# Optimization experiments

Hardware: AMD Instinct MI355X
Metric: run time of the kernel (lower is better)

## Reference

```python
import jax, jax.numpy as jnp
import numpy as np

N = 100_000      # points
F = 64           # feature dim
B = 4            # graphs in batch
POOL_RAD = 0.2   # voxel size
D = 8            # static upper bound on voxels per spatial dim
M_MAX = 1024     # static upper bound on number of nonempty clusters


def setup_inputs() -> dict:
    key = jax.random.key(0)
    k1, k2, k3 = jax.random.split(key, 3)
    pos = jax.random.uniform(k1, (N, 3), dtype=jnp.float32)
    x = jax.random.normal(k2, (N, F), dtype=jnp.float32)
    batch = jnp.sort(jax.random.randint(k3, (N,), 0, B)).astype(jnp.int32)
    return {"pos": pos, "x": x, "batch": batch}


def reference(pos, x, batch):
    batch = batch.astype(jnp.int32)
    rad = jnp.asarray(POOL_RAD, pos.dtype)
    # --- voxel_grid clustering (start = min - rad/2 as in the torch module) ---
    start = pos.min(axis=0) - rad * 0.5
    coords = jnp.clip(jnp.floor((pos - start) / rad).astype(jnp.int32), 0, D - 1)  # [N,3]
    vox = ((batch * D + coords[:, 0]) * D + coords[:, 1]) * D + coords[:, 2]       # [N]
    V = B * D * D * D
    # --- consecutive_cluster + scatter mean of positions ---
    ones = jnp.ones((pos.shape[0],), pos.dtype)
    counts = jax.ops.segment_sum(ones, vox, num_segments=V)       # [V]
    sum_pos = jax.ops.segment_sum(pos, vox, num_segments=V)       # [V,3]
    nonempty = counts > 0
    # compact nonempty voxels to static M_MAX slots (padding duplicates voxel idx 0;
    # argmin tie-breaking to the first index keeps duplicates inert)
    idx = jnp.nonzero(nonempty, size=M_MAX, fill_value=0)[0]      # [M_MAX]
    valid = jnp.arange(M_MAX) < jnp.sum(nonempty)                 # [M_MAX]
    centroids = sum_pos[idx] / jnp.maximum(counts[idx], 1.0)[:, None]  # [M_MAX,3]
    new_batch = idx // (D * D * D)                                # [M_MAX]
    # --- nearest: assign each point to nearest cluster centroid in same graph ---
    d2 = (jnp.sum(pos * pos, axis=1)[:, None]
          - 2.0 * pos @ centroids.T
          + jnp.sum(centroids * centroids, axis=1)[None, :])      # [N, M_MAX]
    big = jnp.asarray(1e30, pos.dtype)
    d2 = jnp.where((batch[:, None] == new_batch[None, :]) & valid[None, :], d2, big)
    assign = jnp.argmin(d2, axis=1)                               # [N]
    # --- scatter max of features into clusters (empty clusters -> 0, as in PyG) ---
    x_pool = jax.ops.segment_max(x, assign, num_segments=M_MAX)   # [M_MAX, F]
    x_pool = jnp.where(jnp.isfinite(x_pool), x_pool, jnp.zeros_like(x_pool))
    return x_pool, centroids, new_batch, valid
```

## Files before the change

kernel.cpp:

```cpp
#include <hip/hip_runtime.h>
#include <stdint.h>

#define DGRID 8
#define NVOX  2048
#define NBATCH 4
#define MMAX  1024
#define FDIM  64
#define CHUNKP 256
#define GRP   20

__device__ __forceinline__ unsigned encf(float f){
  unsigned u = __float_as_uint(f);
  return (u & 0x80000000u) ? ~u : (u | 0x80000000u);
}
__device__ __forceinline__ float decf(unsigned e){
  unsigned u = (e & 0x80000000u) ? (e ^ 0x80000000u) : ~e;
  return __uint_as_float(u);
}


__global__ __launch_bounds__(256) void k_minpart(const float* __restrict__ pos,
    int N, unsigned* __restrict__ bmin, int* __restrict__ counts,
    int* __restrict__ clustCnt, int* __restrict__ clustRank){
  if (blockIdx.x < 8) counts[blockIdx.x * 256 + threadIdx.x] = 0;
  else if (blockIdx.x < 12) clustCnt[(blockIdx.x - 8) * 256 + threadIdx.x] = 0;
  else if (blockIdx.x < 16) clustRank[(blockIdx.x - 12) * 256 + threadIdx.x] = 0;
  unsigned m0 = 0xFFFFFFFFu, m1 = 0xFFFFFFFFu, m2 = 0xFFFFFFFFu;
  int stride = gridDim.x * blockDim.x;
  for (int i = blockIdx.x * blockDim.x + threadIdx.x; i < N; i += stride){
    unsigned e0 = encf(pos[3*i+0]); if (e0 < m0) m0 = e0;
    unsigned e1 = encf(pos[3*i+1]); if (e1 < m1) m1 = e1;
    unsigned e2 = encf(pos[3*i+2]); if (e2 < m2) m2 = e2;
  }
  #pragma unroll
  for (int off = 32; off > 0; off >>= 1){
    unsigned t0 = __shfl_down(m0, off); if (t0 < m0) m0 = t0;
    unsigned t1 = __shfl_down(m1, off); if (t1 < m1) m1 = t1;
    unsigned t2 = __shfl_down(m2, off); if (t2 < m2) m2 = t2;
  }
  __shared__ unsigned sm[4][3];
  int wv = threadIdx.x >> 6, lane = threadIdx.x & 63;
  if (lane == 0){ sm[wv][0] = m0; sm[wv][1] = m1; sm[wv][2] = m2; }
  __syncthreads();
  if (threadIdx.x == 0){
    unsigned a0 = sm[0][0], a1 = sm[0][1], a2 = sm[0][2];
    for (int k = 1; k < 4; k++){
      if (sm[k][0] < a0) a0 = sm[k][0];
      if (sm[k][1] < a1) a1 = sm[k][1];
      if (sm[k][2] < a2) a2 = sm[k][2];
    }
    bmin[blockIdx.x*3+0] = a0;
    bmin[blockIdx.x*3+1] = a1;
    bmin[blockIdx.x*3+2] = a2;
  }
}

__global__ __launch_bounds__(256) void k_vox_hist(const float* __restrict__ pos,
    const int* __restrict__ batch, int N, const unsigned* __restrict__ bmin,
    int* __restrict__ vox, int* __restrict__ chunkHist){
  __shared__ int h[NVOX];
  __shared__ unsigned smin[3];
  for (int t = threadIdx.x; t < NVOX; t += 256) h[t] = 0;
  if (threadIdx.x < 64){
    unsigned a0 = bmin[threadIdx.x*3+0];
    unsigned a1 = bmin[threadIdx.x*3+1];
    unsigned a2 = bmin[threadIdx.x*3+2];
    #pragma unroll
    for (int off = 32; off > 0; off >>= 1){
      unsigned t0 = __shfl_down(a0, off); if (t0 < a0) a0 = t0;
      unsigned t1 = __shfl_down(a1, off); if (t1 < a1) a1 = t1;
      unsigned t2 = __shfl_down(a2, off); if (t2 < a2) a2 = t2;
    }
    if (threadIdx.x == 0){ smin[0] = a0; smin[1] = a1; smin[2] = a2; }
  }
  __syncthreads();
  int c = blockIdx.x;
  int i = c * CHUNKP + threadIdx.x;
  if (i < N){
    float s0 = __fsub_rn(decf(smin[0]), 0.1f);
    float s1 = __fsub_rn(decf(smin[1]), 0.1f);
    float s2 = __fsub_rn(decf(smin[2]), 0.1f);
    float q0 = __fdiv_rn(__fsub_rn(pos[3*i+0], s0), 0.2f);
    float q1 = __fdiv_rn(__fsub_rn(pos[3*i+1], s1), 0.2f);
    float q2 = __fdiv_rn(__fsub_rn(pos[3*i+2], s2), 0.2f);
    int c0 = (int)floorf(q0); c0 = c0 < 0 ? 0 : (c0 > DGRID-1 ? DGRID-1 : c0);
    int c1 = (int)floorf(q1); c1 = c1 < 0 ? 0 : (c1 > DGRID-1 ? DGRID-1 : c1);
    int c2 = (int)floorf(q2); c2 = c2 < 0 ? 0 : (c2 > DGRID-1 ? DGRID-1 : c2);
    int v = ((batch[i]*DGRID + c0)*DGRID + c1)*DGRID + c2;
    vox[i] = v;
    atomicAdd(&h[v], 1);
  }
  __syncthreads();
  for (int t = threadIdx.x; t < NVOX; t += 256)
    chunkHist[c * NVOX + t] = h[t];
}

__global__ __launch_bounds__(256) void k_gsum(int nchunks, int ngroups,
    const int* __restrict__ chunkHist, int* __restrict__ gsum){
  int g = blockIdx.x >> 3;
  int v = (blockIdx.x & 7) * 256 + threadIdx.x;
  if (g >= ngroups) return;
  int c0 = g * GRP, c1 = min(nchunks, c0 + GRP);
  int s = 0;
  for (int c = c0; c < c1; c++) s += chunkHist[c * NVOX + v];
  gsum[g * NVOX + v] = s;
}

__global__ __launch_bounds__(256) void k_gscan(int ngroups,
    int* __restrict__ gsum, int* __restrict__ counts){
  int v = blockIdx.x * 256 + threadIdx.x;
  if (v >= NVOX) return;
  int run = 0;
  for (int g = 0; g < ngroups; g++){
    int t = gsum[g * NVOX + v];
    gsum[g * NVOX + v] = run;
    run += t;
  }
  counts[v] = run;
}

__global__ __launch_bounds__(256) void k_scatter(const float* __restrict__ pos,
    const int* __restrict__ vox, int N, const int* __restrict__ chunkHist,
    const int* __restrict__ gsum, const int* __restrict__ counts,
    int* Mout, int* batchStartC, int* __restrict__ idxOfCluster,
    int* __restrict__ voxBaseG, float* __restrict__ pos_sorted){
  __shared__ int sBase[NVOX];
  __shared__ int rowCnt[4][NVOX];
  int c = blockIdx.x;
  int wv = threadIdx.x >> 6, lane = threadIdx.x & 63;
  if (wv == 0){
    int cs[32];
    int ne = 0, tot = 0;
    #pragma unroll
    for (int j = 0; j < 32; j++){
      int cc2 = counts[lane*32 + j];
      cs[j] = cc2; ne += (cc2 > 0) ? 1 : 0; tot += cc2;
    }
    int inc = ne, incT = tot;
    #pragma unroll
    for (int off = 1; off < 64; off <<= 1){
      int t  = __shfl_up(inc,  off);
      int tt = __shfl_up(incT, off);
      if (lane >= off){ inc += t; incT += tt; }
    }
    int exne = inc - ne, exT = incT - tot;
    int run = exne, bb = exT;
    #pragma unroll
    for (int j = 0; j < 32; j++){
      sBase[lane*32 + j] = bb;
      if (c == 0) voxBaseG[lane*32 + j] = bb;
      bb += cs[j];
      if (cs[j] > 0){
        if (c == 0 && run < MMAX) idxOfCluster[run] = lane*32 + j;
        run++;
      }
    }
    if (c == 0){
      int M = __shfl(run, 63);
      for (int m = M + lane; m < MMAX; m += 64) idxOfCluster[m] = 0;
      int ex0  = __shfl(exne, 0),  ex16 = __shfl(exne, 16);
      int ex32 = __shfl(exne, 32), ex48 = __shfl(exne, 48);
      if (lane == 0){
        Mout[0] = M;
        batchStartC[0] = ex0;  batchStartC[1] = ex16;
        batchStartC[2] = ex32; batchStartC[3] = ex48;
        batchStartC[NBATCH] = (M < MMAX) ? M : MMAX;
      }
    }
  } else {
    for (int t = threadIdx.x - 64; t < 4*NVOX; t += 192)
      ((int*)rowCnt)[t] = 0;
  }
  __syncthreads();
  {
    int g = c / GRP, cg0 = g * GRP;
    for (int t = threadIdx.x; t < NVOX; t += 256){
      int b = sBase[t] + gsum[g * NVOX + t];
      for (int cc = cg0; cc < c; cc++) b += chunkHist[cc * NVOX + t];
      sBase[t] = b;
    }
  }
  __syncthreads();
  int i = c * CHUNKP + threadIdx.x;
  bool valid = i < N;
  int v = valid ? vox[i] : -1;
  float px = 0.f, py = 0.f, pz = 0.f;
  if (valid){ px = pos[3*i+0]; py = pos[3*i+1]; pz = pos[3*i+2]; }
  int rank = 0, cnt = 0;
  #pragma unroll 8
  for (int j = 0; j < 64; j++){
    int vj = __shfl(v, j);
    if (vj == v){
      cnt++;
      if (j < lane) rank++;
    }
  }
  if (valid && rank == 0) rowCnt[wv][v] = cnt;
  __syncthreads();
  if (valid){
    int pre = 0;
    for (int rr = 0; rr < wv; rr++) pre += rowCnt[rr][v];
    int dst = sBase[v] + pre + rank;
    pos_sorted[3*dst+0] = px;
    pos_sorted[3*dst+1] = py;
    pos_sorted[3*dst+2] = pz;
  }
}

__global__ __launch_bounds__(64) void k_sum2cent(const float* __restrict__ pos_sorted,
    const int* __restrict__ voxBase, const int* __restrict__ counts,
    float4* __restrict__ centv){
  int v = blockIdx.x * 64 + threadIdx.x;
  if (v >= NVOX) return;
  int lo = voxBase[v], cnt = counts[v];
  const float* p = pos_sorted + 3*(size_t)lo;
  float sx = 0.f, sy = 0.f, sz = 0.f;
  int k = 0;
  for (; k + 4 <= cnt; k += 4){
    float a0 = p[0],  a1 = p[1],  a2 = p[2];
    float b0 = p[3],  b1 = p[4],  b2 = p[5];
    float c0 = p[6],  c1 = p[7],  c2 = p[8];
    float d0 = p[9],  d1 = p[10], d2 = p[11];
    sx = __fadd_rn(__fadd_rn(__fadd_rn(__fadd_rn(sx, a0), b0), c0), d0);
    sy = __fadd_rn(__fadd_rn(__fadd_rn(__fadd_rn(sy, a1), b1), c1), d1);
    sz = __fadd_rn(__fadd_rn(__fadd_rn(__fadd_rn(sz, a2), b2), c2), d2);
    p += 12;
  }
  for (; k < cnt; k++){
    sx = __fadd_rn(sx, p[0]);
    sy = __fadd_rn(sy, p[1]);
    sz = __fadd_rn(sz, p[2]);
    p += 3;
  }
  float den = fmaxf((float)cnt, 1.0f);
  float cx = __fdiv_rn(sx, den);
  float cy = __fdiv_rn(sy, den);
  float cz = __fdiv_rn(sz, den);
  float c2 = __fadd_rn(__fadd_rn(__fmul_rn(cx,cx), __fmul_rn(cy,cy)), __fmul_rn(cz,cz));
  centv[v] = make_float4(cx, cy, cz, c2);
}

__global__ __launch_bounds__(256) void k_argmin2(const float* __restrict__ pos,
    const int* __restrict__ batch, int N, const float4* __restrict__ centv,
    const int* __restrict__ idxOfCluster, const int* __restrict__ Mout,
    const int* __restrict__ batchStartC, int* __restrict__ assign,
    int* __restrict__ clustCnt, float* __restrict__ outC,
    float* __restrict__ outNB, float* __restrict__ outValid){
  __shared__ float4 sc[MMAX];
  __shared__ int h[MMAX];
  for (int m = threadIdx.x; m < MMAX; m += 256){
    sc[m] = centv[idxOfCluster[m]];
    h[m] = 0;
  }
  __syncthreads();
  if (blockIdx.x == 0){
    int M = Mout[0];
    for (int m = threadIdx.x; m < MMAX; m += 256){
      float4 cc = sc[m];
      outC[3*m+0] = cc.x; outC[3*m+1] = cc.y; outC[3*m+2] = cc.z;
      outNB[m] = (float)(idxOfCluster[m] >> 9);
      outValid[m] = (m < M) ? 1.0f : 0.0f;
    }
  }
  int i = blockIdx.x * 256 + threadIdx.x;
  if (i < N){
    float px = pos[3*i+0], py = pos[3*i+1], pz = pos[3*i+2];
    float p2 = __fadd_rn(__fadd_rn(__fmul_rn(px,px), __fmul_rn(py,py)), __fmul_rn(pz,pz));
    int b = batch[i];
    int mlo = batchStartC[b], mhi = batchStartC[b+1];
    float best = 3.402823466e+38f;
    int bm = mlo;
    for (int m = mlo; m < mhi; m++){
      float4 cc = sc[m];
      float dot = __fadd_rn(__fadd_rn(__fmul_rn(px,cc.x), __fmul_rn(py,cc.y)),
                            __fmul_rn(pz,cc.z));
      float d2  = __fadd_rn(__fsub_rn(p2, __fmul_rn(2.0f, dot)), cc.w);
      if (d2 < best){ best = d2; bm = m; }
    }
    assign[i] = bm;
    atomicAdd(&h[bm], 1);
  }
  __syncthreads();
  for (int t = threadIdx.x; t < MMAX; t += 256){
    int c = h[t];
    if (c > 0) atomicAdd(&clustCnt[t], c);
  }
}

__global__ __launch_bounds__(256) void k_scatter2s(const int* __restrict__ assign,
    int N, const int* __restrict__ clustCnt, int* __restrict__ clustRank,
    int* __restrict__ clustBaseG, int* __restrict__ idx_sorted){
  __shared__ int cb[MMAX];
  int wv = threadIdx.x >> 6, lane = threadIdx.x & 63;
  if (wv == 0){
    int cs[16]; int tot = 0;
    #pragma unroll
    for (int j = 0; j < 16; j++){ cs[j] = clustCnt[lane*16 + j]; tot += cs[j]; }
    int inc = tot;
    #pragma unroll
    for (int off = 1; off < 64; off <<= 1){
      int t = __shfl_up(inc, off);
      if (lane >= off) inc += t;
    }
    int bb = inc - tot;
    #pragma unroll
    for (int j = 0; j < 16; j++){
      cb[lane*16 + j] = bb;
      if (blockIdx.x == 0) clustBaseG[lane*16 + j] = bb;
      bb += cs[j];
    }
  }
  __syncthreads();
  int i = blockIdx.x * 256 + threadIdx.x;
  if (i >= N) return;
  int m = assign[i];
  int r = atomicAdd(&clustRank[m], 1);
  idx_sorted[cb[m] + r] = i;
}

__global__ __launch_bounds__(256) void k_xmax(const float* __restrict__ x,
    const int* __restrict__ idx_sorted, const int* __restrict__ clustBase,
    const int* __restrict__ clustCnt, float* __restrict__ outX){
  int w = blockIdx.x * 4 + (threadIdx.x >> 6);
  int lane = threadIdx.x & 63;
  if (w >= MMAX) return;
  int lo = clustBase[w], cnt = clustCnt[w];
  float mx = -3.402823466e+38f;
  int k = 0;
  for (; k + 4 <= cnt; k += 4){
    int r0 = idx_sorted[lo+k+0], r1 = idx_sorted[lo+k+1];
    int r2 = idx_sorted[lo+k+2], r3 = idx_sorted[lo+k+3];
    float a = x[(size_t)r0 * FDIM + lane];
    float b = x[(size_t)r1 * FDIM + lane];
    float c = x[(size_t)r2 * FDIM + lane];
    float d = x[(size_t)r3 * FDIM + lane];
    mx = fmaxf(mx, fmaxf(fmaxf(a, b), fmaxf(c, d)));
  }
  for (; k < cnt; k++){
    int r0 = idx_sorted[lo+k];
    mx = fmaxf(mx, x[(size_t)r0 * FDIM + lane]);
  }
  outX[w * FDIM + lane] = (cnt > 0) ? mx : 0.0f;
}


__global__ __launch_bounds__(256) void k_init(unsigned* startEnc, int* batchCnt){
  int t = threadIdx.x;
  if (t < 3) startEnc[t] = 0xFFFFFFFFu;
  if (t < NBATCH) batchCnt[t] = 0;
}

__global__ __launch_bounds__(256) void k_min_hist(const float* __restrict__ pos,
    const int* __restrict__ batch, int N, unsigned* startEnc, int* batchCnt){
  __shared__ int sbin[NBATCH];
  if (threadIdx.x < NBATCH) sbin[threadIdx.x] = 0;
  __syncthreads();
  unsigned m0 = 0xFFFFFFFFu, m1 = 0xFFFFFFFFu, m2 = 0xFFFFFFFFu;
  int stride = gridDim.x * blockDim.x;
  for (int i = blockIdx.x * blockDim.x + threadIdx.x; i < N; i += stride){
    unsigned e0 = encf(pos[3*i+0]); if (e0 < m0) m0 = e0;
    unsigned e1 = encf(pos[3*i+1]); if (e1 < m1) m1 = e1;
    unsigned e2 = encf(pos[3*i+2]); if (e2 < m2) m2 = e2;
    atomicAdd(&sbin[batch[i]], 1);
  }
  #pragma unroll
  for (int off = 32; off > 0; off >>= 1){
    unsigned t0 = __shfl_down(m0, off); if (t0 < m0) m0 = t0;
    unsigned t1 = __shfl_down(m1, off); if (t1 < m1) m1 = t1;
    unsigned t2 = __shfl_down(m2, off); if (t2 < m2) m2 = t2;
  }
  if ((threadIdx.x & 63) == 0){
    atomicMin(&startEnc[0], m0);
    atomicMin(&startEnc[1], m1);
    atomicMin(&startEnc[2], m2);
  }
  __syncthreads();
  if (threadIdx.x < NBATCH) atomicAdd(&batchCnt[threadIdx.x], sbin[threadIdx.x]);
}

__global__ __launch_bounds__(256) void k_vox(const float* __restrict__ pos,
    const int* __restrict__ batch, int N, const unsigned* __restrict__ startEnc,
    int* __restrict__ vox, int* __restrict__ counts){
  int i = blockIdx.x * blockDim.x + threadIdx.x;
  if (i >= N) return;
  float s0 = __fsub_rn(decf(startEnc[0]), 0.1f);
  float s1 = __fsub_rn(decf(startEnc[1]), 0.1f);
  float s2 = __fsub_rn(decf(startEnc[2]), 0.1f);
  float q0 = __fdiv_rn(__fsub_rn(pos[3*i+0], s0), 0.2f);
  float q1 = __fdiv_rn(__fsub_rn(pos[3*i+1], s1), 0.2f);
  float q2 = __fdiv_rn(__fsub_rn(pos[3*i+2], s2), 0.2f);
  int c0 = (int)floorf(q0); c0 = c0 < 0 ? 0 : (c0 > DGRID-1 ? DGRID-1 : c0);
  int c1 = (int)floorf(q1); c1 = c1 < 0 ? 0 : (c1 > DGRID-1 ? DGRID-1 : c1);
  int c2 = (int)floorf(q2); c2 = c2 < 0 ? 0 : (c2 > DGRID-1 ? DGRID-1 : c2);
  int v = ((batch[i]*DGRID + c0)*DGRID + c1)*DGRID + c2;
  vox[i] = v;
  atomicAdd(&counts[v], 1);
}

__global__ __launch_bounds__(64) void k_scan_old(const int* __restrict__ counts,
    const int* __restrict__ batchCnt, int* batchPtr, int* Mout,
    int* batchStartC, int* __restrict__ idxOfCluster, int* __restrict__ voxBase){
  int lane = threadIdx.x;
  int cs[32];
  int ne = 0, tot = 0;
  #pragma unroll
  for (int j = 0; j < 32; j++){
    int c = counts[lane*32 + j];
    cs[j] = c;
    ne += (c > 0) ? 1 : 0;
    tot += c;
  }
  int inc = ne, incT = tot;
  #pragma unroll
  for (int off = 1; off < 64; off <<= 1){
    int t  = __shfl_up(inc,  off);
    int tt = __shfl_up(incT, off);
    if (lane >= off){ inc += t; incT += tt; }
  }
  int exne = inc - ne;
  int bb   = incT - tot;
  int run = exne;
  #pragma unroll
  for (int j = 0; j < 32; j++){
    voxBase[lane*32 + j] = bb;
    bb += cs[j];
    if (cs[j] > 0){
      if (run < MMAX) idxOfCluster[run] = lane*32 + j;
      run++;
    }
  }
  int M = __shfl(run, 63);
  for (int m = M + lane; m < MMAX; m += 64) idxOfCluster[m] = 0;
  int ex0  = __shfl(exne, 0);
  int ex16 = __shfl(exne, 16);
  int ex32 = __shfl(exne, 32);
  int ex48 = __shfl(exne, 48);
  if (lane == 0){
    Mout[0] = M;
    int acc = 0;
    for (int b = 0; b < NBATCH; b++){ batchPtr[b] = acc; acc += batchCnt[b]; }
    batchPtr[NBATCH] = acc;
    batchStartC[0] = ex0;  batchStartC[1] = ex16;
    batchStartC[2] = ex32; batchStartC[3] = ex48;
    batchStartC[NBATCH] = (M < MMAX) ? M : MMAX;
  }
}

__global__ __launch_bounds__(64) void k_sum(const float* __restrict__ pos,
    const int* __restrict__ vox, const int* __restrict__ counts,
    const int* __restrict__ batchPtr, float* __restrict__ sum_pos){
  int v = blockIdx.x * 64 + threadIdx.x;
  if (v >= NVOX) return;
  int b = v >> 9;
  int lo = batchPtr[b], hi = batchPtr[b+1];
  float sx = 0.f, sy = 0.f, sz = 0.f;
  if (counts[v] > 0){
    for (int i = lo; i < hi; i++){
      if (vox[i] == v){
        sx = __fadd_rn(sx, pos[3*i+0]);
        sy = __fadd_rn(sy, pos[3*i+1]);
        sz = __fadd_rn(sz, pos[3*i+2]);
      }
    }
  }
  sum_pos[3*v+0] = sx;
  sum_pos[3*v+1] = sy;
  sum_pos[3*v+2] = sz;
}

__global__ __launch_bounds__(256) void k_cent(const float* __restrict__ sum_pos,
    const int* __restrict__ counts, const int* __restrict__ idxOfCluster,
    const int* __restrict__ Mout, float4* __restrict__ cent4,
    float* __restrict__ outC, float* __restrict__ outNB, float* __restrict__ outValid){
  int m = blockIdx.x * blockDim.x + threadIdx.x;
  if (m >= MMAX) return;
  int M = Mout[0];
  int v = idxOfCluster[m];
  float den = fmaxf((float)counts[v], 1.0f);
  float cx = __fdiv_rn(sum_pos[3*v+0], den);
  float cy = __fdiv_rn(sum_pos[3*v+1], den);
  float cz = __fdiv_rn(sum_pos[3*v+2], den);
  float c2 = __fadd_rn(__fadd_rn(__fmul_rn(cx,cx), __fmul_rn(cy,cy)), __fmul_rn(cz,cz));
  cent4[m] = make_float4(cx, cy, cz, c2);
  outC[3*m+0] = cx; outC[3*m+1] = cy; outC[3*m+2] = cz;
  outNB[m] = (float)(v >> 9);
  outValid[m] = (m < M) ? 1.0f : 0.0f;
}

__global__ __launch_bounds__(256) void k_assign_slow(const float* __restrict__ pos,
    const float* __restrict__ x, const int* __restrict__ batch, int N,
    const float4* __restrict__ cent4, const int* __restrict__ batchStartC,
    unsigned* __restrict__ encMax){
  __shared__ float4 sc[MMAX];
  for (int m = threadIdx.x; m < MMAX; m += blockDim.x) sc[m] = cent4[m];
  __syncthreads();
  int i = blockIdx.x * blockDim.x + threadIdx.x;
  if (i >= N) return;
  float px = pos[3*i+0], py = pos[3*i+1], pz = pos[3*i+2];
  float p2 = __fadd_rn(__fadd_rn(__fmul_rn(px,px), __fmul_rn(py,py)), __fmul_rn(pz,pz));
  int b = batch[i];
  int mlo = batchStartC[b], mhi = batchStartC[b+1];
  float best = 3.402823466e+38f;
  int bm = mlo;
  for (int m = mlo; m < mhi; m++){
    float4 c = sc[m];
    float dot = __fadd_rn(__fadd_rn(__fmul_rn(px,c.x), __fmul_rn(py,c.y)),
                          __fmul_rn(pz,c.z));
    float d2  = __fadd_rn(__fsub_rn(p2, __fmul_rn(2.0f, dot)), c.w);
    if (d2 < best){ best = d2; bm = m; }
  }
  unsigned* dst = encMax + bm * FDIM;
  const float4* xi = (const float4*)(x + (size_t)i * FDIM);
  #pragma unroll
  for (int f4 = 0; f4 < FDIM/4; f4++){
    float4 xv = xi[f4];
    atomicMax(&dst[4*f4+0], encf(xv.x));
    atomicMax(&dst[4*f4+1], encf(xv.y));
    atomicMax(&dst[4*f4+2], encf(xv.z));
    atomicMax(&dst[4*f4+3], encf(xv.w));
  }
}
__global__ __launch_bounds__(256) void k_decode(const unsigned* __restrict__ encMax,
    float* __restrict__ outX){
  int t = blockIdx.x * blockDim.x + threadIdx.x;
  if (t >= MMAX * FDIM) return;
  unsigned e = encMax[t];
  outX[t] = (e == 0u) ? 0.0f : decf(e);
}


extern "C" void kernel_launch(void* const* d_in, const int* in_sizes, int n_in,
                              void* d_out, int out_size, void* d_ws, size_t ws_size,
                              hipStream_t stream){
  const float* pos   = (const float*)d_in[0];
  const float* x     = (const float*)d_in[1];
  const int*   batch = (const int*)d_in[2];
  const int N = in_sizes[2];

  char* w = (char*)d_ws;
  unsigned* bmin         = (unsigned*)(w + 0);
  unsigned* startEnc     = (unsigned*)(w + 768);
  int*      batchCnt     = (int*)(w + 784);
  int*      batchPtr     = (int*)(w + 800);
  int*      Mout         = (int*)(w + 832);
  int*      batchStartC  = (int*)(w + 848);
  int*      counts       = (int*)(w + 896);
  int*      voxBaseG     = (int*)(w + 9088);
  float*    sum_pos      = (float*)(w + 17280);
  int*      idxOfCluster = (int*)(w + 41856);
  float4*   cent4        = (float4*)(w + 45952);
  int*      clustCnt     = (int*)(w + 62336);
  int*      clustBaseG   = (int*)(w + 66432);
  int*      clustRank    = (int*)(w + 70528);
  float4*   centv        = (float4*)(w + 74624);
  unsigned* encMax       = (unsigned*)(w + 107392);
  int*      gsum         = (int*)(w + 107392);
  int*      vox          = (int*)(w + 369536);
  size_t voxEnd = 369536 + (size_t)N * 4;
  size_t chOff  = (voxEnd + 15) & ~(size_t)15;

  int nchunks = (N + CHUNKP - 1) / CHUNKP;
  int ngroups = (nchunks + GRP - 1) / GRP;
  size_t psOff = chOff + (size_t)nchunks * NVOX * 4;
  size_t need  = psOff + (size_t)N * 3 * 4;
  const bool fast = (ws_size >= need) && (ngroups <= 32);

  int*   chunkHist  = (int*)(w + chOff);
  float* pos_sorted = (float*)(w + psOff);
  int* assign     = (int*)pos_sorted;
  int* idx_sorted = (int*)pos_sorted + N;

  float* outX     = (float*)d_out;
  float* outC     = outX + MMAX * FDIM;
  float* outNB    = outC + MMAX * 3;
  float* outValid = outNB + MMAX;

  const int nb = (N + 255) / 256;
  if (fast){
    k_minpart<<<64, 256, 0, stream>>>(pos, N, bmin, counts, clustCnt, clustRank);
    k_vox_hist<<<nchunks, 256, 0, stream>>>(pos, batch, N, bmin, vox, chunkHist);
    k_gsum<<<ngroups * 8, 256, 0, stream>>>(nchunks, ngroups, chunkHist, gsum);
    k_gscan<<<NVOX / 256, 256, 0, stream>>>(ngroups, gsum, counts);
    k_scatter<<<nchunks, 256, 0, stream>>>(pos, vox, N, chunkHist, gsum, counts,
                                           Mout, batchStartC, idxOfCluster,
                                           voxBaseG, pos_sorted);
    k_sum2cent<<<NVOX / 64, 64, 0, stream>>>(pos_sorted, voxBaseG, counts, centv);
    k_argmin2<<<nb, 256, 0, stream>>>(pos, batch, N, centv, idxOfCluster, Mout,
                                      batchStartC, assign, clustCnt,
                                      outC, outNB, outValid);
    k_scatter2s<<<nb, 256, 0, stream>>>(assign, N, clustCnt, clustRank,
                                        clustBaseG, idx_sorted);
    k_xmax<<<MMAX / 4, 256, 0, stream>>>(x, idx_sorted, clustBaseG, clustCnt, outX);
  } else {
    k_init<<<1, 256, 0, stream>>>(startEnc, batchCnt);
    hipMemsetAsync(counts, 0, NVOX * 4, stream);
    hipMemsetAsync(encMax, 0, MMAX * FDIM * 4, stream);
    k_min_hist<<<256, 256, 0, stream>>>(pos, batch, N, startEnc, batchCnt);
    k_vox<<<nb, 256, 0, stream>>>(pos, batch, N, startEnc, vox, counts);
    k_scan_old<<<1, 64, 0, stream>>>(counts, batchCnt, batchPtr, Mout, batchStartC,
                                     idxOfCluster, voxBaseG);
    k_sum<<<(NVOX + 63) / 64, 64, 0, stream>>>(pos, vox, counts, batchPtr, sum_pos);
    k_cent<<<MMAX / 256, 256, 0, stream>>>(sum_pos, counts, idxOfCluster, Mout,
                                           cent4, outC, outNB, outValid);
    k_assign_slow<<<nb, 256, 0, stream>>>(pos, x, batch, N, cent4, batchStartC, encMax);
    k_decode<<<(MMAX * FDIM + 255) / 256, 256, 0, stream>>>(encMax, outX);
  }
}
```

Measured before the change: 149.6 us.

## Recompute voxel ids in scatter and fold group scan into gsum atomics

Drops the per-point vox array: the histogram kernel no longer writes it, and the scatter kernel recomputes voxel indices from pos, batch and the partial minima. The separate k_gscan launch is removed. k_gsum now accumulates total counts with global atomics, and each scatter block sums the preceding group totals itself. This removes one kernel launch and a round trip of N ints through global memory, at the cost of duplicated voxel arithmetic and an O(ngroups) loop per voxel in every scatter block. It relies on counts being zeroed by k_minpart before k_gsum runs.

```diff
diff --git a/kernel.cpp b/kernel.cpp
--- a/kernel.cpp
+++ b/kernel.cpp
@@ -55,9 +55,9 @@
   }
 }
 
-__global__ __launch_bounds__(256) void k_vox_hist(const float* __restrict__ pos,
+__global__ __launch_bounds__(256) void k_chist(const float* __restrict__ pos,
     const int* __restrict__ batch, int N, const unsigned* __restrict__ bmin,
-    int* __restrict__ vox, int* __restrict__ chunkHist){
+    int* __restrict__ chunkHist){
   __shared__ int h[NVOX];
   __shared__ unsigned smin[3];
   for (int t = threadIdx.x; t < NVOX; t += 256) h[t] = 0;
@@ -87,7 +87,6 @@
     int c1 = (int)floorf(q1); c1 = c1 < 0 ? 0 : (c1 > DGRID-1 ? DGRID-1 : c1);
     int c2 = (int)floorf(q2); c2 = c2 < 0 ? 0 : (c2 > DGRID-1 ? DGRID-1 : c2);
     int v = ((batch[i]*DGRID + c0)*DGRID + c1)*DGRID + c2;
-    vox[i] = v;
     atomicAdd(&h[v], 1);
   }
   __syncthreads();
@@ -96,7 +95,8 @@
 }
 
 __global__ __launch_bounds__(256) void k_gsum(int nchunks, int ngroups,
-    const int* __restrict__ chunkHist, int* __restrict__ gsum){
+    const int* __restrict__ chunkHist, int* __restrict__ gsum,
+    int* __restrict__ counts){
   int g = blockIdx.x >> 3;
   int v = (blockIdx.x & 7) * 256 + threadIdx.x;
   if (g >= ngroups) return;
@@ -104,28 +104,18 @@
   int s = 0;
   for (int c = c0; c < c1; c++) s += chunkHist[c * NVOX + v];
   gsum[g * NVOX + v] = s;
-}
-
-__global__ __launch_bounds__(256) void k_gscan(int ngroups,
-    int* __restrict__ gsum, int* __restrict__ counts){
-  int v = blockIdx.x * 256 + threadIdx.x;
-  if (v >= NVOX) return;
-  int run = 0;
-  for (int g = 0; g < ngroups; g++){
-    int t = gsum[g * NVOX + v];
-    gsum[g * NVOX + v] = run;
-    run += t;
-  }
-  counts[v] = run;
+  if (s > 0) atomicAdd(&counts[v], s);
 }
 
 __global__ __launch_bounds__(256) void k_scatter(const float* __restrict__ pos,
-    const int* __restrict__ vox, int N, const int* __restrict__ chunkHist,
+    const int* __restrict__ batch, int N, const int* __restrict__ chunkHist,
     const int* __restrict__ gsum, const int* __restrict__ counts,
+    const unsigned* __restrict__ bmin,
     int* Mout, int* batchStartC, int* __restrict__ idxOfCluster,
     int* __restrict__ voxBaseG, float* __restrict__ pos_sorted){
   __shared__ int sBase[NVOX];
   __shared__ int rowCnt[4][NVOX];
+  __shared__ unsigned smin[3];
   int c = blockIdx.x;
   int wv = threadIdx.x >> 6, lane = threadIdx.x & 63;
   if (wv == 0){
@@ -168,6 +158,18 @@
       }
     }
   } else {
+    if (wv == 1){
+      unsigned a0 = bmin[lane*3+0];
+      unsigned a1 = bmin[lane*3+1];
+      unsigned a2 = bmin[lane*3+2];
+      #pragma unroll
+      for (int off = 32; off > 0; off >>= 1){
+        unsigned t0 = __shfl_down(a0, off); if (t0 < a0) a0 = t0;
+        unsigned t1 = __shfl_down(a1, off); if (t1 < a1) a1 = t1;
+        unsigned t2 = __shfl_down(a2, off); if (t2 < a2) a2 = t2;
+      }
+      if (lane == 0){ smin[0] = a0; smin[1] = a1; smin[2] = a2; }
+    }
     for (int t = threadIdx.x - 64; t < 4*NVOX; t += 192)
       ((int*)rowCnt)[t] = 0;
   }
@@ -175,7 +177,8 @@
   {
     int g = c / GRP, cg0 = g * GRP;
     for (int t = threadIdx.x; t < NVOX; t += 256){
-      int b = sBase[t] + gsum[g * NVOX + t];
+      int b = sBase[t];
+      for (int gg = 0; gg < g; gg++) b += gsum[gg * NVOX + t];
       for (int cc = cg0; cc < c; cc++) b += chunkHist[cc * NVOX + t];
       sBase[t] = b;
     }
@@ -183,9 +186,21 @@
   __syncthreads();
   int i = c * CHUNKP + threadIdx.x;
   bool valid = i < N;
-  int v = valid ? vox[i] : -1;
+  int v = -1;
   float px = 0.f, py = 0.f, pz = 0.f;
-  if (valid){ px = pos[3*i+0]; py = pos[3*i+1]; pz = pos[3*i+2]; }
+  if (valid){
+    px = pos[3*i+0]; py = pos[3*i+1]; pz = pos[3*i+2];
+    float s0 = __fsub_rn(decf(smin[0]), 0.1f);
+    float s1 = __fsub_rn(decf(smin[1]), 0.1f);
+    float s2 = __fsub_rn(decf(smin[2]), 0.1f);
+    float q0 = __fdiv_rn(__fsub_rn(px, s0), 0.2f);
+    float q1 = __fdiv_rn(__fsub_rn(py, s1), 0.2f);
+    float q2 = __fdiv_rn(__fsub_rn(pz, s2), 0.2f);
+    int c0 = (int)floorf(q0); c0 = c0 < 0 ? 0 : (c0 > DGRID-1 ? DGRID-1 : c0);
+    int c1 = (int)floorf(q1); c1 = c1 < 0 ? 0 : (c1 > DGRID-1 ? DGRID-1 : c1);
+    int c2 = (int)floorf(q2); c2 = c2 < 0 ? 0 : (c2 > DGRID-1 ? DGRID-1 : c2);
+    v = ((batch[i]*DGRID + c0)*DGRID + c1)*DGRID + c2;
+  }
   int rank = 0, cnt = 0;
   #pragma unroll 8
   for (int j = 0; j < 64; j++){
@@ -578,11 +593,10 @@
   const int nb = (N + 255) / 256;
   if (fast){
     k_minpart<<<64, 256, 0, stream>>>(pos, N, bmin, counts, clustCnt, clustRank);
-    k_vox_hist<<<nchunks, 256, 0, stream>>>(pos, batch, N, bmin, vox, chunkHist);
-    k_gsum<<<ngroups * 8, 256, 0, stream>>>(nchunks, ngroups, chunkHist, gsum);
-    k_gscan<<<NVOX / 256, 256, 0, stream>>>(ngroups, gsum, counts);
-    k_scatter<<<nchunks, 256, 0, stream>>>(pos, vox, N, chunkHist, gsum, counts,
-                                           Mout, batchStartC, idxOfCluster,
+    k_chist<<<nchunks, 256, 0, stream>>>(pos, batch, N, bmin, chunkHist);
+    k_gsum<<<ngroups * 8, 256, 0, stream>>>(nchunks, ngroups, chunkHist, gsum, counts);
+    k_scatter<<<nchunks, 256, 0, stream>>>(pos, batch, N, chunkHist, gsum, counts,
+                                           bmin, Mout, batchStartC, idxOfCluster,
                                            voxBaseG, pos_sorted);
     k_sum2cent<<<NVOX / 64, 64, 0, stream>>>(pos_sorted, voxBaseG, counts, centv);
     k_argmin2<<<nb, 256, 0, stream>>>(pos, batch, N, centv, idxOfCluster, Mout,
```

Result: slower. 154.4 us (+3.2%).
